# Kernel tuning notes

Hardware: AMD Instinct MI355X
Metric: run time of the kernel (lower is better)

Reference implementation:

```python
import jax, jax.numpy as jnp
import numpy as np

B, S, D, H = 2, 2048, 1024, 16
HD = D // H  # head dim = 64

def setup_inputs() -> dict:
    key = jax.random.key(0)
    ks = jax.random.split(key, 11)
    s = 0.02
    return {
        "query": jax.random.normal(ks[0], (B, S, D), jnp.float32),
        "key_in": jax.random.normal(ks[1], (B, S, D), jnp.float32),
        "value": jax.random.normal(ks[2], (B, S, D), jnp.float32),
        "Wq": jax.random.normal(ks[3], (D, D), jnp.float32) * s,
        "bq": jnp.zeros((D,), jnp.float32),
        "Wk": jax.random.normal(ks[4], (D, D), jnp.float32) * s,
        "bk": jnp.zeros((D,), jnp.float32),
        "Wv": jax.random.normal(ks[5], (D, D), jnp.float32) * s,
        "bv": jnp.zeros((D,), jnp.float32),
        "Wo": jax.random.normal(ks[6], (D, D), jnp.float32) * s,
        "bo": jnp.zeros((D,), jnp.float32),
    }

def _split_heads(x):
    b, s, _ = x.shape
    return x.reshape(b, s, H, HD).transpose(0, 2, 1, 3)  # [B,H,S,HD]

def reference(query, key_in, value, Wq, bq, Wk, bk, Wv, bv, Wo, bo):
    q = _split_heads(query @ Wq + bq)
    k = _split_heads(key_in @ Wk + bk)
    v = _split_heads(value @ Wv + bv)
    scores = jnp.einsum("bhqd,bhkd->bhqk", q, k) / jnp.sqrt(jnp.float32(HD))
    weights = jax.nn.softmax(scores, axis=-1)  # dropout = identity (eval)
    ctx = jnp.einsum("bhqk,bhkd->bhqd", weights, v)
    ctx = ctx.transpose(0, 2, 1, 3).reshape(query.shape[0], -1, D)
    return ctx @ Wo + bo
```

## Files before the change

kernel.cpp:

```cpp
#include <hip/hip_runtime.h>
#include <hip/hip_bf16.h>


typedef __attribute__((ext_vector_type(8))) short short8;
typedef __attribute__((ext_vector_type(4))) short short4v;
typedef __attribute__((ext_vector_type(4))) float f32x4;

static __device__ __forceinline__ short f2bf(float f) {
    union { float f; unsigned u; } c; c.f = f;
    unsigned r = c.u + 0x7fff + ((c.u >> 16) & 1);
    return (short)(r >> 16);
}

static __device__ __forceinline__ unsigned pk_bf16(float a, float b) {
    union { __hip_bfloat162 h; unsigned u; } c;
    c.h = __float22bfloat162_rn(make_float2(a, b));
    return c.u;
}

typedef const void __attribute__((address_space(1)))* gas_ptr;
typedef void __attribute__((address_space(3)))* las_ptr;
static __device__ __forceinline__ void gload16(const void* g, void* l) {
    __builtin_amdgcn_global_load_lds((gas_ptr)g, (las_ptr)l, 16, 0, 0);
}

__global__ __launch_bounds__(256) void prep(
    const float* __restrict__ X0, const float* __restrict__ X1,
    const float* __restrict__ X2, short* __restrict__ Abf,
    const float* __restrict__ W0, const float* __restrict__ W1,
    const float* __restrict__ W2, const float* __restrict__ W3,
    short* __restrict__ Wt)
{
    __shared__ float tile[32][33];
    const int bid = blockIdx.x;
    if (bid < 6144) {
        const int zz = bid >> 11, xb = bid & 2047;
        const float* X = zz == 0 ? X0 : zz == 1 ? X1 : X2;
        short* o = Abf + ((size_t)zz << 22);
        const int i = (xb * 256 + threadIdx.x) * 8;
        const float4 a = *(const float4*)(X + i);
        const float4 b = *(const float4*)(X + i + 4);
        uint4 r;
        r.x = pk_bf16(a.x, a.y); r.y = pk_bf16(a.z, a.w);
        r.z = pk_bf16(b.x, b.y); r.w = pk_bf16(b.z, b.w);
        *(uint4*)(o + i) = r;
    } else {
        const int wid = bid - 6144;
        const int z = wid >> 10;
        const float* W = z == 0 ? W0 : z == 1 ? W1 : z == 2 ? W2 : W3;
        short* O = Wt + ((size_t)z << 20);
        const int k0 = (wid & 31) * 32, n0 = ((wid >> 5) & 31) * 32;
        const int tx = threadIdx.x & 31, ty = threadIdx.x >> 5;
        #pragma unroll
        for (int j = 0; j < 32; j += 8)
            tile[ty + j][tx] = W[(k0 + ty + j) * 1024 + n0 + tx];
        __syncthreads();
        #pragma unroll
        for (int j = 0; j < 32; j += 8)
            O[(n0 + ty + j) * 1024 + k0 + tx] = f2bf(tile[tx][ty + j]);
    }
}

__global__ __launch_bounds__(256, 3) void gemmqkv(
    const short* __restrict__ Abase, const short* __restrict__ Wt,
    const float* __restrict__ bq, const float* __restrict__ bk,
    const float* __restrict__ bv, short* __restrict__ Qh,
    short* __restrict__ Kh, short* __restrict__ Vt, float qscale)
{
    __shared__ short Al[2][4096];
    __shared__ short Bl[2][4096];
    const int flat = blockIdx.z * 256 + blockIdx.y * 8 + blockIdx.x;
    const int remap = (flat & 7) * 96 + (flat >> 3);
    const int z = remap >> 8;
    const int rem = remap & 255;
    const int m0 = (rem >> 3) * 128, n0 = (rem & 7) * 128;

    const short* Aa = Abase + ((size_t)z << 22);
    const short* Ba = Wt + ((size_t)z << 20);
    const float* bias = z == 0 ? bq : z == 1 ? bk : bv;
    short* O = z == 0 ? Qh : z == 1 ? Kh : Vt;
    const float scale = z == 0 ? qscale : 1.0f;

    const int t = threadIdx.x;
    const int lane = t & 63, w = t >> 6;
    const int lm = lane & 15, lg = lane >> 4;
    const int wr = w >> 1, wc = w & 1;

    #define STAGEQ(buf, k0) do {                                              \
        _Pragma("unroll")                                                     \
        for (int j = 0; j < 2; ++j) {                                         \
            const int c = j * 256 + t;                                        \
            gload16(Aa + (size_t)(m0 + (c >> 2)) * 1024 + (k0) + (c & 3) * 8, \
                    &Al[buf][j * 2048 + w * 512]);                            \
            gload16(Ba + (size_t)(n0 + (c >> 2)) * 1024 + (k0) + (c & 3) * 8, \
                    &Bl[buf][j * 2048 + w * 512]);                            \
        }                                                                     \
    } while (0)

    f32x4 acc[4][4] = {};
    STAGEQ(0, 0);
    __syncthreads();

    int buf = 0;
    for (int kk = 0; kk < 32; ++kk) {
        if (kk < 31) STAGEQ(buf ^ 1, (kk + 1) * 32);
        const short* Ab = Al[buf];
        const short* Bb = Bl[buf];
        short8 af[4], bfr[4];
        #pragma unroll
        for (int mf = 0; mf < 4; ++mf)
            af[mf] = *(const short8*)(Ab + (wr * 64 + mf * 16 + lm) * 32 + lg * 8);
        #pragma unroll
        for (int nf = 0; nf < 4; ++nf)
            bfr[nf] = *(const short8*)(Bb + (wc * 64 + nf * 16 + lm) * 32 + lg * 8);
        #pragma unroll
        for (int mf = 0; mf < 4; ++mf)
            #pragma unroll
            for (int nf = 0; nf < 4; ++nf)
                acc[mf][nf] = __builtin_amdgcn_mfma_f32_16x16x32_bf16(
                    af[mf], bfr[nf], acc[mf][nf], 0, 0, 0);
        __syncthreads();
        buf ^= 1;
    }
    #undef STAGEQ

    #pragma unroll
    for (int mf = 0; mf < 4; ++mf) {
        const int mb = m0 + wr * 64 + mf * 16 + lg * 4;
        #pragma unroll
        for (int nf = 0; nf < 4; ++nf) {
            const int n = n0 + wc * 64 + nf * 16 + lm;
            const float bs = bias[n];
            if (z == 2) {
                short4v sv;
                #pragma unroll
                for (int i = 0; i < 4; ++i)
                    sv[i] = f2bf(acc[mf][nf][i] + bs);
                const int addr = (((mb >> 11) * 16 + (n >> 6)) * 64 + (n & 63)) * 2048 + (mb & 2047);
                *(short4v*)&O[addr] = sv;
            } else {
                #pragma unroll
                for (int i = 0; i < 4; ++i) {
                    const int m = mb + i;
                    const int addr = (((m >> 11) * 16 + (n >> 6)) * 2048 + (m & 2047)) * 64 + (n & 63);
                    O[addr] = f2bf(scale * (acc[mf][nf][i] + bs));
                }
            }
        }
    }
}

#define STAGE(buf, k0) do {                                                   \
    gload16(Aa + (size_t)(gm0 + (t >> 2)) * 1024 + (k0) + (t & 3) * 8,        \
            &Al[buf][w * 512]);                                               \
    _Pragma("unroll")                                                         \
    for (int j = 0; j < 2; ++j) {                                             \
        const int c = j * 256 + t;                                            \
        gload16(Ba + (size_t)(gn0 + (c >> 2)) * 1024 + (k0) + (c & 3) * 8,    \
                &Bl[buf][j * 2048 + w * 512]);                                \
    }                                                                         \
} while (0)

#define GEMM_CORE(Aa_, Ba_, m0v, n0v)                                         \
    __shared__ short Al[2][2048];                           \
    __shared__ short Bl[2][4096];                          \
    const int t = threadIdx.x;                                                \
    const int gm0 = (m0v), gn0 = (n0v);                                       \
    const int lane = t & 63, w = t >> 6;                                      \
    const int lm = lane & 15, lg = lane >> 4;                                 \
    const int wr = w >> 1, wc = w & 1;                                        \
    f32x4 acc[2][4] = {};                                                     \
    STAGE(0, 0);                                                              \
    __syncthreads();                                                          \
    int buf = 0;                                                              \
    for (int kk = 0; kk < 32; ++kk) {                                         \
        if (kk < 31) STAGE(buf ^ 1, (kk + 1) * 32);                           \
        const short* Ab = Al[buf];                                            \
        const short* Bb = Bl[buf];                                            \
        short8 af[2], bfr[4];                                                 \
        _Pragma("unroll")                                                     \
        for (int mf = 0; mf < 2; ++mf)                                        \
            af[mf] = *(const short8*)(Ab + (wr * 32 + mf * 16 + lm) * 32 + lg * 8); \
        _Pragma("unroll")                                                     \
        for (int nf = 0; nf < 4; ++nf)                                        \
            bfr[nf] = *(const short8*)(Bb + (wc * 64 + nf * 16 + lm) * 32 + lg * 8); \
        _Pragma("unroll")                                                     \
        for (int mf = 0; mf < 2; ++mf)                                        \
            _Pragma("unroll")                                                 \
            for (int nf = 0; nf < 4; ++nf)                                    \
                acc[mf][nf] = __builtin_amdgcn_mfma_f32_16x16x32_bf16(        \
                    af[mf], bfr[nf], acc[mf][nf], 0, 0, 0);                   \
        __syncthreads();                                                      \
        buf ^= 1;                                                             \
    }

__global__ __launch_bounds__(256) void gemmo(
    const short* __restrict__ Aa, const short* __restrict__ Ba,
    const float* __restrict__ bias, float* __restrict__ Out)
{
    const int flat = blockIdx.y * 8 + blockIdx.x;
    const int remap = (flat & 7) * 64 + (flat >> 3);
    const int m0 = (remap >> 3) * 64, n0 = (remap & 7) * 128;

    GEMM_CORE(Aa, Ba, m0, n0)

    #pragma unroll
    for (int mf = 0; mf < 2; ++mf) {
        const int mb = m0 + wr * 32 + mf * 16 + lg * 4;
        #pragma unroll
        for (int nf = 0; nf < 4; ++nf) {
            const int n = n0 + wc * 64 + nf * 16 + lm;
            const float bs = bias[n];
            #pragma unroll
            for (int i = 0; i < 4; ++i)
                Out[(mb + i) * 1024 + n] = acc[mf][nf][i] + bs;
        }
    }
}
#undef STAGE
#undef GEMM_CORE

__global__ __launch_bounds__(512, 4) void attn_k(
    const short* __restrict__ Q, const short* __restrict__ K,
    const short* __restrict__ V, short* __restrict__ Ctx)
{
    __shared__ short Kl[2][128][64];
    __shared__ short Vl[2][2][64][64];
    __shared__ short Pl[8][16][64];
    const int t = threadIdx.x;
    const int flat = blockIdx.y * 16 + blockIdx.x;
    const int remap = (flat & 7) * 64 + (flat >> 3);
    const int qt = remap & 15, bh = remap >> 4;
    const int lane = t & 63, w = t >> 6;
    const int lm = lane & 15, lg = lane >> 4;
    const int swz = (lm & 7) << 3;
    const int swc = lm & 7;

    const int qrow = qt * 128 + w * 16 + lm;
    short8 qf[2];
    #pragma unroll
    for (int ks = 0; ks < 2; ++ks)
        qf[ks] = *(const short8*)(Q + ((size_t)bh * 2048 + qrow) * 64 + ks * 32 + lg * 8);

    float m_run = -3e38f, l_run = 0.f;
    f32x4 o_acc[4] = {};

    const int rk = t >> 2, ck = t & 3;
    const int rv = t >> 3, cv = t & 7;
    const short* Kg = K + ((size_t)bh * 2048 + rk) * 64 + ck * 16;
    const short* Vg = V + ((size_t)bh * 64 + rv) * 2048 + cv * 16;
    const int koff0 = rk * 64 + ((ck * 2) ^ (rk & 7)) * 8;
    const int koff1 = rk * 64 + ((ck * 2 + 1) ^ (rk & 7)) * 8;
    const int vhalf = (cv >> 2) * 4096;
    const int voff0 = vhalf + rv * 64 + (((cv * 2) & 7) ^ (rv & 7)) * 8;
    const int voff1 = vhalf + rv * 64 + (((cv * 2 + 1) & 7) ^ (rv & 7)) * 8;

    {
        short8 a = *(const short8*)(Kg);
        short8 b = *(const short8*)(Kg + 8);
        short8 c = *(const short8*)(Vg);
        short8 d = *(const short8*)(Vg + 8);
        *(short8*)((short*)Kl[0] + koff0) = a;
        *(short8*)((short*)Kl[0] + koff1) = b;
        *(short8*)((short*)Vl[0] + voff0) = c;
        *(short8*)((short*)Vl[0] + voff1) = d;
    }

    short* prow = &Pl[w][lm][0];
    int cur = 0;

    for (int kt = 0; kt < 16; ++kt) {
        __syncthreads();

        short8 kn0, kn1, vn0, vn1;
        const bool pfn = (kt < 15);
        if (pfn) {
            const short* Kgn = Kg + (size_t)(kt + 1) * 8192;
            const short* Vgn = Vg + (kt + 1) * 128;
            kn0 = *(const short8*)(Kgn);
            kn1 = *(const short8*)(Kgn + 8);
            vn0 = *(const short8*)(Vgn);
            vn1 = *(const short8*)(Vgn + 8);
        }

        const short* Kc = (const short*)Kl[cur];
        const short* Vc = (const short*)Vl[cur];

        f32x4 sa[2][4] = {};
        #pragma unroll
        for (int h = 0; h < 2; ++h)
            #pragma unroll
            for (int nf = 0; nf < 4; ++nf) {
                const int rr = h * 64 + nf * 16 + lm;
                #pragma unroll
                for (int ks = 0; ks < 2; ++ks) {
                    const short8 kf = *(const short8*)(Kc + rr * 64 + ((ks * 4 + lg) ^ swc) * 8);
                    sa[h][nf] = __builtin_amdgcn_mfma_f32_16x16x32_bf16(kf, qf[ks], sa[h][nf], 0, 0, 0);
                }
            }

        float mx[8];
        #pragma unroll
        for (int h = 0; h < 2; ++h)
            #pragma unroll
            for (int nf = 0; nf < 4; ++nf) {
                const f32x4 v = sa[h][nf];
                mx[h * 4 + nf] = fmaxf(fmaxf(v[0], v[1]), fmaxf(v[2], v[3]));
            }
        float mt = fmaxf(fmaxf(fmaxf(mx[0], mx[1]), fmaxf(mx[2], mx[3])),
                         fmaxf(fmaxf(mx[4], mx[5]), fmaxf(mx[6], mx[7])));
        mt = fmaxf(mt, __shfl_xor(mt, 16));
        mt = fmaxf(mt, __shfl_xor(mt, 32));
        if (__any(mt > m_run + 8.0f)) {
            const float mn = fmaxf(m_run, mt);
            const float alpha = exp2f(m_run - mn);
            l_run *= alpha;
            #pragma unroll
            for (int nf = 0; nf < 4; ++nf)
                #pragma unroll
                for (int i = 0; i < 4; ++i)
                    o_acc[nf][i] *= alpha;
            m_run = mn;
        }
        float ps[8];
        #pragma unroll
        for (int h = 0; h < 2; ++h)
            #pragma unroll
            for (int nf = 0; nf < 4; ++nf) {
                f32x4 v = sa[h][nf];
                #pragma unroll
                for (int i = 0; i < 4; ++i) v[i] = exp2f(v[i] - m_run);
                sa[h][nf] = v;
                ps[h * 4 + nf] = (v[0] + v[1]) + (v[2] + v[3]);
            }
        float rs = ((ps[0] + ps[1]) + (ps[2] + ps[3])) +
                   ((ps[4] + ps[5]) + (ps[6] + ps[7]));
        rs += __shfl_xor(rs, 16);
        rs += __shfl_xor(rs, 32);
        l_run += rs;

        #pragma unroll
        for (int h = 0; h < 2; ++h) {
            #pragma unroll
            for (int nf = 0; nf < 4; ++nf) {
                uint2 pv;
                pv.x = pk_bf16(sa[h][nf][0], sa[h][nf][1]);
                pv.y = pk_bf16(sa[h][nf][2], sa[h][nf][3]);
                *(uint2*)(prow + ((nf * 16 + lg * 4) ^ swz)) = pv;
            }
            short8 pf[2];
            #pragma unroll
            for (int ks = 0; ks < 2; ++ks)
                pf[ks] = *(const short8*)(prow + ((ks * 32 + lg * 8) ^ swz));

            if (h == 0 && pfn) {
                short* Kn = (short*)Kl[cur ^ 1];
                short* Vn = (short*)Vl[cur ^ 1];
                *(short8*)(Kn + koff0) = kn0;
                *(short8*)(Kn + koff1) = kn1;
                *(short8*)(Vn + voff0) = vn0;
                *(short8*)(Vn + voff1) = vn1;
            }

            #pragma unroll
            for (int nf = 0; nf < 4; ++nf) {
                const int rr = nf * 16 + lm;
                #pragma unroll
                for (int ks = 0; ks < 2; ++ks) {
                    const short8 vf = *(const short8*)(Vc + h * 4096 + rr * 64 + ((ks * 4 + lg) ^ swc) * 8);
                    o_acc[nf] = __builtin_amdgcn_mfma_f32_16x16x32_bf16(vf, pf[ks], o_acc[nf], 0, 0, 0);
                }
            }
        }
        cur ^= 1;
    }

    const float inv = 1.f / l_run;
    const int b = bh >> 4, h = bh & 15;
    short* outp = Ctx + ((size_t)b * 2048 + qrow) * 1024 + h * 64 + lg * 4;
    #pragma unroll
    for (int nf = 0; nf < 4; ++nf) {
        uint2 pk;
        pk.x = pk_bf16(o_acc[nf][0] * inv, o_acc[nf][1] * inv);
        pk.y = pk_bf16(o_acc[nf][2] * inv, o_acc[nf][3] * inv);
        *(uint2*)(outp + nf * 16) = pk;
    }
}

extern "C" void kernel_launch(void* const* d_in, const int* in_sizes, int n_in,
                              void* d_out, int out_size, void* d_ws, size_t ws_size,
                              hipStream_t stream)
{
    const float* query  = (const float*)d_in[0];
    const float* key_in = (const float*)d_in[1];
    const float* value  = (const float*)d_in[2];
    const float* Wq = (const float*)d_in[3];
    const float* bq = (const float*)d_in[4];
    const float* Wk = (const float*)d_in[5];
    const float* bk = (const float*)d_in[6];
    const float* Wv = (const float*)d_in[7];
    const float* bv = (const float*)d_in[8];
    const float* Wo = (const float*)d_in[9];
    const float* bo = (const float*)d_in[10];
    float* out = (float*)d_out;

    char* ws = (char*)d_ws;
    short* Wt  = (short*)(ws);
    short* Abf = (short*)(ws + (8  << 20));
    short* Qh  = (short*)(ws + (32 << 20));
    short* Kh  = (short*)(ws + (40 << 20));
    short* Vt  = (short*)(ws + (48 << 20));
    short* Ctx = Abf;

    const float qscale = 0.125f * 1.44269504088896f;

    hipLaunchKernelGGL(prep, dim3(10240), dim3(256), 0, stream,
                       query, key_in, value, Abf, Wq, Wk, Wv, Wo, Wt);
    hipLaunchKernelGGL(gemmqkv, dim3(8, 32, 3), dim3(256), 0, stream,
                       Abf, Wt, bq, bk, bv, Qh, Kh, Vt, qscale);
    hipLaunchKernelGGL(attn_k, dim3(16, 32), dim3(512), 0, stream,
                       Qh, Kh, Vt, Ctx);
    hipLaunchKernelGGL(gemmo, dim3(8, 64), dim3(256), 0, stream,
                       Ctx, Wt + (3 << 20), bo, out);
}
```

Measured before the change: 138.1 us.

## Fuse fp32-to-bf16 activation conversion into QKV GEMM operand staging

Removes the separate activation-conversion pass from the prep kernel, which read the three fp32 inputs and wrote bf16 copies to the workspace. The QKV GEMM now loads fp32 A tiles directly into registers for the next K step, runs the current step's MFMAs, then converts and writes bf16 into the other LDS buffer before the barrier. This avoids a full extra global round trip for the activations. In exchange, A loads go through registers instead of async global-to-LDS copies, and each tile re-reads twice as many bytes of fp32 data across column blocks. That adds register pressure and global/L2 traffic inside the GEMM.

```diff
diff --git a/kernel.cpp b/kernel.cpp
--- a/kernel.cpp
+++ b/kernel.cpp
@@ -25,44 +25,29 @@
 }
 
 __global__ __launch_bounds__(256) void prep(
-    const float* __restrict__ X0, const float* __restrict__ X1,
-    const float* __restrict__ X2, short* __restrict__ Abf,
     const float* __restrict__ W0, const float* __restrict__ W1,
     const float* __restrict__ W2, const float* __restrict__ W3,
     short* __restrict__ Wt)
 {
     __shared__ float tile[32][33];
-    const int bid = blockIdx.x;
-    if (bid < 6144) {
-        const int zz = bid >> 11, xb = bid & 2047;
-        const float* X = zz == 0 ? X0 : zz == 1 ? X1 : X2;
-        short* o = Abf + ((size_t)zz << 22);
-        const int i = (xb * 256 + threadIdx.x) * 8;
-        const float4 a = *(const float4*)(X + i);
-        const float4 b = *(const float4*)(X + i + 4);
-        uint4 r;
-        r.x = pk_bf16(a.x, a.y); r.y = pk_bf16(a.z, a.w);
-        r.z = pk_bf16(b.x, b.y); r.w = pk_bf16(b.z, b.w);
-        *(uint4*)(o + i) = r;
-    } else {
-        const int wid = bid - 6144;
-        const int z = wid >> 10;
-        const float* W = z == 0 ? W0 : z == 1 ? W1 : z == 2 ? W2 : W3;
-        short* O = Wt + ((size_t)z << 20);
-        const int k0 = (wid & 31) * 32, n0 = ((wid >> 5) & 31) * 32;
-        const int tx = threadIdx.x & 31, ty = threadIdx.x >> 5;
-        #pragma unroll
-        for (int j = 0; j < 32; j += 8)
-            tile[ty + j][tx] = W[(k0 + ty + j) * 1024 + n0 + tx];
-        __syncthreads();
-        #pragma unroll
-        for (int j = 0; j < 32; j += 8)
-            O[(n0 + ty + j) * 1024 + k0 + tx] = f2bf(tile[tx][ty + j]);
-    }
+    const int wid = blockIdx.x;
+    const int z = wid >> 10;
+    const float* W = z == 0 ? W0 : z == 1 ? W1 : z == 2 ? W2 : W3;
+    short* O = Wt + ((size_t)z << 20);
+    const int k0 = (wid & 31) * 32, n0 = ((wid >> 5) & 31) * 32;
+    const int tx = threadIdx.x & 31, ty = threadIdx.x >> 5;
+    #pragma unroll
+    for (int j = 0; j < 32; j += 8)
+        tile[ty + j][tx] = W[(k0 + ty + j) * 1024 + n0 + tx];
+    __syncthreads();
+    #pragma unroll
+    for (int j = 0; j < 32; j += 8)
+        O[(n0 + ty + j) * 1024 + k0 + tx] = f2bf(tile[tx][ty + j]);
 }
 
 __global__ __launch_bounds__(256, 3) void gemmqkv(
-    const short* __restrict__ Abase, const short* __restrict__ Wt,
+    const float* __restrict__ Xq, const float* __restrict__ Xk,
+    const float* __restrict__ Xv, const short* __restrict__ Wt,
     const float* __restrict__ bq, const float* __restrict__ bk,
     const float* __restrict__ bv, short* __restrict__ Qh,
     short* __restrict__ Kh, short* __restrict__ Vt, float qscale)
@@ -75,7 +60,7 @@
     const int rem = remap & 255;
     const int m0 = (rem >> 3) * 128, n0 = (rem & 7) * 128;
 
-    const short* Aa = Abase + ((size_t)z << 22);
+    const float* Af = z == 0 ? Xq : z == 1 ? Xk : Xv;
     const short* Ba = Wt + ((size_t)z << 20);
     const float* bias = z == 0 ? bq : z == 1 ? bk : bv;
     short* O = z == 0 ? Qh : z == 1 ? Kh : Vt;
@@ -86,24 +71,52 @@
     const int lm = lane & 15, lg = lane >> 4;
     const int wr = w >> 1, wc = w & 1;
 
-    #define STAGEQ(buf, k0) do {                                              \
+    const float* Ag0 = Af + (size_t)(m0 + (t >> 2)) * 1024 + (t & 3) * 8;
+    const float* Ag1 = Ag0 + (size_t)64 * 1024;
+    short* const ad0[2] = { &Al[0][t * 8],        &Al[1][t * 8]        };
+    short* const ad1[2] = { &Al[0][2048 + t * 8], &Al[1][2048 + t * 8] };
+
+    #define STAGEB(buf, k0) do {                                              \
         _Pragma("unroll")                                                     \
         for (int j = 0; j < 2; ++j) {                                         \
             const int c = j * 256 + t;                                        \
-            gload16(Aa + (size_t)(m0 + (c >> 2)) * 1024 + (k0) + (c & 3) * 8, \
-                    &Al[buf][j * 2048 + w * 512]);                            \
             gload16(Ba + (size_t)(n0 + (c >> 2)) * 1024 + (k0) + (c & 3) * 8, \
                     &Bl[buf][j * 2048 + w * 512]);                            \
         }                                                                     \
     } while (0)
+    #define CVT8(dst, va, vb) do {                                            \
+        uint4 r_;                                                             \
+        r_.x = pk_bf16((va).x, (va).y); r_.y = pk_bf16((va).z, (va).w);       \
+        r_.z = pk_bf16((vb).x, (vb).y); r_.w = pk_bf16((vb).z, (vb).w);       \
+        *(uint4*)(dst) = r_;                                                  \
+    } while (0)
 
     f32x4 acc[4][4] = {};
-    STAGEQ(0, 0);
+
+    {
+        float4 a00 = *(const float4*)(Ag0);
+        float4 a01 = *(const float4*)(Ag0 + 4);
+        float4 a10 = *(const float4*)(Ag1);
+        float4 a11 = *(const float4*)(Ag1 + 4);
+        STAGEB(0, 0);
+        CVT8(ad0[0], a00, a01);
+        CVT8(ad1[0], a10, a11);
+    }
     __syncthreads();
 
     int buf = 0;
     for (int kk = 0; kk < 32; ++kk) {
-        if (kk < 31) STAGEQ(buf ^ 1, (kk + 1) * 32);
+        float4 a00, a01, a10, a11;
+        const bool pfn = (kk < 31);
+        if (pfn) {
+            const int kn = (kk + 1) * 32;
+            a00 = *(const float4*)(Ag0 + kn);
+            a01 = *(const float4*)(Ag0 + kn + 4);
+            a10 = *(const float4*)(Ag1 + kn);
+            a11 = *(const float4*)(Ag1 + kn + 4);
+            STAGEB(buf ^ 1, kn);
+        }
+
         const short* Ab = Al[buf];
         const short* Bb = Bl[buf];
         short8 af[4], bfr[4];
@@ -119,10 +132,16 @@
             for (int nf = 0; nf < 4; ++nf)
                 acc[mf][nf] = __builtin_amdgcn_mfma_f32_16x16x32_bf16(
                     af[mf], bfr[nf], acc[mf][nf], 0, 0, 0);
+
+        if (pfn) {
+            CVT8(ad0[buf ^ 1], a00, a01);
+            CVT8(ad1[buf ^ 1], a10, a11);
+        }
         __syncthreads();
         buf ^= 1;
     }
-    #undef STAGEQ
+    #undef STAGEB
+    #undef CVT8
 
     #pragma unroll
     for (int mf = 0; mf < 4; ++mf) {
@@ -406,18 +425,17 @@
 
     char* ws = (char*)d_ws;
     short* Wt  = (short*)(ws);
-    short* Abf = (short*)(ws + (8  << 20));
+    short* Ctx = (short*)(ws + (8  << 20));
     short* Qh  = (short*)(ws + (32 << 20));
     short* Kh  = (short*)(ws + (40 << 20));
     short* Vt  = (short*)(ws + (48 << 20));
-    short* Ctx = Abf;
 
     const float qscale = 0.125f * 1.44269504088896f;
 
-    hipLaunchKernelGGL(prep, dim3(10240), dim3(256), 0, stream,
-                       query, key_in, value, Abf, Wq, Wk, Wv, Wo, Wt);
+    hipLaunchKernelGGL(prep, dim3(4096), dim3(256), 0, stream,
+                       Wq, Wk, Wv, Wo, Wt);
     hipLaunchKernelGGL(gemmqkv, dim3(8, 32, 3), dim3(256), 0, stream,
-                       Abf, Wt, bq, bk, bv, Qh, Kh, Vt, qscale);
+                       query, key_in, value, Wt, bq, bk, bv, Qh, Kh, Vt, qscale);
     hipLaunchKernelGGL(attn_k, dim3(16, 32), dim3(512), 0, stream,
                        Qh, Kh, Vt, Ctx);
     hipLaunchKernelGGL(gemmo, dim3(8, 64), dim3(256), 0, stream,
```

After: 139.2 us. Within noise of the previous version (+0.8%).
